# Kernel optimization log

Measured on AMD Instinct MI355X. Metric: run time of the kernel, lower is better.

The kernel has to match this reference:

```python
import jax, jax.numpy as jnp
import numpy as np


def _bilinear_sample(im, pt):
    """torch.nn.functional.grid_sample(im[None], pt[None,None], align_corners=False),
    bilinear, zeros padding.  im: (C,H,W); pt: (N,2) with (x,y) in [-1,1].
    Returns (C, N)."""
    C, H, W = im.shape
    # align_corners=False unnormalization
    x = ((pt[:, 0] + 1.0) * W - 1.0) * 0.5
    y = ((pt[:, 1] + 1.0) * H - 1.0) * 0.5
    x0 = jnp.floor(x)
    y0 = jnp.floor(y)
    wx1 = x - x0
    wy1 = y - y0
    wx0 = 1.0 - wx1
    wy0 = 1.0 - wy1
    x0i = x0.astype(jnp.int32)
    y0i = y0.astype(jnp.int32)

    def gather(xi, yi):
        inb = ((xi >= 0) & (xi < W) & (yi >= 0) & (yi < H)).astype(im.dtype)
        v = im[:, jnp.clip(yi, 0, H - 1), jnp.clip(xi, 0, W - 1)]  # (C, N)
        return v * inb

    return (gather(x0i, y0i) * (wx0 * wy0)
            + gather(x0i + 1, y0i) * (wx1 * wy0)
            + gather(x0i, y0i + 1) * (wx0 * wy1)
            + gather(x0i + 1, y0i + 1) * (wx1 * wy1))


def setup_inputs() -> dict:
    key = jax.random.key(0)
    H = W = 2048
    N = 262144
    k1, k2, k3 = jax.random.split(key, 3)
    dP = jax.random.normal(k1, (2, H, W), dtype=jnp.float32)
    inds = jnp.stack([jax.random.randint(k2, (N,), 0, H),
                      jax.random.randint(k3, (N,), 0, W)]).astype(jnp.int32)
    return {"dP": dP, "inds": inds, "niter": 60}


def reference(dP, inds, niter):
    # Faithful jax port of follow_flows + set_pt (cellpose flow integration).
    ndim, H, W = dP.shape
    # img_size_minus_1, indexed per channel k as in the original code
    sizes = jnp.array([H - 1, W - 1], dtype=jnp.float32)
    # im[0, ndim-1-n] = dP[n]; then im[:, k] *= 2 / sizes[k]
    im = dP[::-1] * (2.0 / sizes)[:, None, None]  # (2, H, W)
    # pt[..., ndim-1-n] = inds[n]  ->  pt[:, 0] = x = inds[1], pt[:, 1] = y = inds[0]
    pt0 = jnp.stack([inds[1].astype(jnp.float32),
                     inds[0].astype(jnp.float32)], axis=-1)  # (N, 2)
    pt0 = pt0 / sizes[None, :] * 2.0 - 1.0

    def step(pt, _):
        dPt = _bilinear_sample(im, pt)                 # (2, N); channel k adds to pt[..., k]
        return jnp.clip(pt + dPt.T, -1.0, 1.0), None

    pt, _ = jax.lax.scan(step, pt0, None, length=niter)
    pt = (pt + 1.0) * 0.5 * sizes[None, :]
    # return pt[..., [1, 0]].squeeze().T  -> (2, N): row0 = y, row1 = x
    return pt[:, ::-1].T
```

## Files before the change

kernel.cpp:

```cpp
#include <hip/hip_runtime.h>

#define TILE_SHIFT 5
#define NXCD 8

__global__ __launch_bounds__(256) void interleave_kernel(
    const float* __restrict__ dP, float2* __restrict__ im,
    int HW, float s0, float s1, int swz_on)
{
    int bid = blockIdx.x;
    if (swz_on) {
        int cpx = gridDim.x >> 3;
        bid = (bid & (NXCD - 1)) * cpx + (bid >> 3);
    }
    int i = bid * blockDim.x + threadIdx.x;
    int nquad = HW >> 2;
    if (i >= nquad) return;
    const float4* p0 = reinterpret_cast<const float4*>(dP);
    const float4* p1 = reinterpret_cast<const float4*>(dP + HW);
    float4 a = p1[i];
    float4 b = p0[i];
    float4 lo, hi;
    lo.x = a.x * s0; lo.y = b.x * s1; lo.z = a.y * s0; lo.w = b.y * s1;
    hi.x = a.z * s0; hi.y = b.z * s1; hi.z = a.w * s0; hi.w = b.w * s1;
    float4* outv = reinterpret_cast<float4*>(im);
    outv[2 * i]     = lo;
    outv[2 * i + 1] = hi;
}

__global__ __launch_bounds__(256) void zero_kernel(int* __restrict__ p, int n)
{
    int i = blockIdx.x * blockDim.x + threadIdx.x;
    if (i < n) p[i] = 0;
}

__device__ __forceinline__ int point_tile(const int* inds, int n, int N,
                                          int H, int W, int tiles_x)
{
    int y = inds[n];
    int x = inds[N + n];
    int ty = min(max(y, 0), H - 1) >> TILE_SHIFT;
    int tx = min(max(x, 0), W - 1) >> TILE_SHIFT;
    return ty * tiles_x + tx;
}

__global__ __launch_bounds__(256) void hist_kernel(
    const int* __restrict__ inds, int* __restrict__ hist,
    int N, int H, int W, int tiles_x)
{
    int n = blockIdx.x * blockDim.x + threadIdx.x;
    if (n >= N) return;
    atomicAdd(&hist[point_tile(inds, n, N, H, W, tiles_x)], 1);
}

__global__ __launch_bounds__(1024) void scan_kernel(
    const int* __restrict__ hist, int* __restrict__ cursor, int ntiles)
{
    __shared__ int partial[1024];
    const int tid = threadIdx.x;
    const int items = (ntiles + 1023) >> 10;
    const int base = tid * items;
    int sum = 0;
    for (int i = 0; i < items; ++i) {
        int idx = base + i;
        if (idx < ntiles) sum += hist[idx];
    }
    partial[tid] = sum;
    __syncthreads();
    for (int off = 1; off < 1024; off <<= 1) {
        int v = (tid >= off) ? partial[tid - off] : 0;
        __syncthreads();
        partial[tid] += v;
        __syncthreads();
    }
    int excl = (tid == 0) ? 0 : partial[tid - 1];
    for (int i = 0; i < items; ++i) {
        int idx = base + i;
        if (idx < ntiles) {
            int h = hist[idx];
            cursor[idx] = excl;
            excl += h;
        }
    }
}

__global__ __launch_bounds__(256) void scatter_kernel(
    const int* __restrict__ inds, int* __restrict__ cursor,
    int* __restrict__ perm, int N, int H, int W, int tiles_x)
{
    int n = blockIdx.x * blockDim.x + threadIdx.x;
    if (n >= N) return;
    int slot = atomicAdd(&cursor[point_tile(inds, n, N, H, W, tiles_x)], 1);
    perm[slot] = n;
}

template <int MODE>
__global__ __launch_bounds__(256) void iterate1_kernel(
    const float2* __restrict__ im, const float* __restrict__ dP,
    const int* __restrict__ perm,
    const int* __restrict__ inds, const int* __restrict__ niter_p,
    float* __restrict__ out, int H, int W, int N, int swz_on)
{
#pragma clang fp contract(off)
    int bid = blockIdx.x;
    if (swz_on) {
        int cpx = gridDim.x >> 3;
        bid = (bid & (NXCD - 1)) * cpx + (bid >> 3);
    }
    const int t = bid * blockDim.x + threadIdx.x;
    if (t >= N) return;
    const int niter = niter_p[0];
    const float sH = (float)(H - 1);
    const float sW = (float)(W - 1);
    const float s0 = 2.0f / sH;
    const float s1 = 2.0f / sW;
    const int HW = H * W;
    const float Wf = (float)W, Hf = (float)H;

    const int pid = (MODE == 2) ? perm[t] : t;

    float px = ((float)inds[N + pid] / sH) * 2.0f - 1.0f;
    float py = ((float)inds[pid]     / sW) * 2.0f - 1.0f;

    for (int it = 0; it < niter; ++it) {
        float x = ((px + 1.0f) * Wf - 1.0f) * 0.5f;
        float y = ((py + 1.0f) * Hf - 1.0f) * 0.5f;
        float x0f = floorf(x), y0f = floorf(y);
        float wx1 = x - x0f,  wy1 = y - y0f;
        float wx0 = 1.0f - wx1, wy0 = 1.0f - wy1;
        int x0 = (int)x0f, y0 = (int)y0f;
        int x1 = x0 + 1,   y1 = y0 + 1;

        int x0c = min(max(x0, 0), W - 1);
        int x1c = min(max(x1, 0), W - 1);
        int y0c = min(max(y0, 0), H - 1);
        int y1c = min(max(y1, 0), H - 1);
        bool bx0 = (x0 >= 0) & (x0 < W);
        bool bx1 = (x1 >= 0) & (x1 < W);
        bool by0 = (y0 >= 0) & (y0 < H);
        bool by1 = (y1 >= 0) & (y1 < H);

        float2 v00, v10, v01, v11;
        if (MODE >= 1) {
            const float2* r0 = im + (size_t)y0c * W;
            const float2* r1 = im + (size_t)y1c * W;
            v00 = r0[x0c]; v10 = r0[x1c];
            v01 = r1[x0c]; v11 = r1[x1c];
        } else {
            int i00 = y0c * W + x0c, i10 = y0c * W + x1c;
            int i01 = y1c * W + x0c, i11 = y1c * W + x1c;
            v00 = make_float2(dP[HW + i00] * s0, dP[i00] * s1);
            v10 = make_float2(dP[HW + i10] * s0, dP[i10] * s1);
            v01 = make_float2(dP[HW + i01] * s0, dP[i01] * s1);
            v11 = make_float2(dP[HW + i11] * s0, dP[i11] * s1);
        }
        const float2 zero = make_float2(0.0f, 0.0f);
        if (!(bx0 & by0)) v00 = zero;
        if (!(bx1 & by0)) v10 = zero;
        if (!(bx0 & by1)) v01 = zero;
        if (!(bx1 & by1)) v11 = zero;

        float w00 = wx0 * wy0, w10 = wx1 * wy0;
        float w01 = wx0 * wy1, w11 = wx1 * wy1;
        float dx = ((v00.x * w00 + v10.x * w10) + v01.x * w01) + v11.x * w11;
        float dy = ((v00.y * w00 + v10.y * w10) + v01.y * w01) + v11.y * w11;

        px = fminf(fmaxf(px + dx, -1.0f), 1.0f);
        py = fminf(fmaxf(py + dy, -1.0f), 1.0f);
    }

    out[pid]     = (py + 1.0f) * 0.5f * sW;
    out[N + pid] = (px + 1.0f) * 0.5f * sH;
}

extern "C" void kernel_launch(void* const* d_in, const int* in_sizes, int n_in,
                              void* d_out, int out_size, void* d_ws, size_t ws_size,
                              hipStream_t stream) {
    const float* dP      = (const float*)d_in[0];
    const int*   inds    = (const int*)d_in[1];
    const int*   niter_p = (const int*)d_in[2];
    float*       out     = (float*)d_out;

    const int HW = in_sizes[0] / 2;
    int W = 1;
    while ((long long)W * W < (long long)HW) W <<= 1;
    const int H = HW / W;
    const int N = in_sizes[1] / 2;

    const float s0 = 2.0f / (float)(H - 1);
    const float s1 = 2.0f / (float)(W - 1);

    const int tiles_x = ((W - 1) >> TILE_SHIFT) + 1;
    const int tiles_y = ((H - 1) >> TILE_SHIFT) + 1;
    const int ntiles  = tiles_x * tiles_y;

    const size_t im_bytes   = (size_t)HW * sizeof(float2);
    const size_t perm_bytes = (size_t)N * sizeof(int);
    const size_t aux_bytes  = (size_t)2 * ntiles * sizeof(int);

    char* base = (char*)d_ws;
    float2* im     = (float2*)base;
    int*    perm   = (int*)(base + im_bytes);
    int*    hist   = (int*)(base + im_bytes + perm_bytes);
    int*    cursor = hist + ntiles;

    const int nblkN  = (N + 255) / 256;
    const int nblkIm = (HW / 4 + 255) / 256;
    const int swzIm  = (nblkIm % NXCD) == 0 && (HW / 4) % 256 == 0;
    const int swzIt  = (nblkN % NXCD) == 0 && (N % 256) == 0;

    if (ws_size >= im_bytes + perm_bytes + aux_bytes) {
        interleave_kernel<<<nblkIm, 256, 0, stream>>>(
            dP, im, HW, s0, s1, swzIm);
        zero_kernel<<<(ntiles + 255) / 256, 256, 0, stream>>>(hist, ntiles);
        hist_kernel<<<nblkN, 256, 0, stream>>>(inds, hist, N, H, W, tiles_x);
        scan_kernel<<<1, 1024, 0, stream>>>(hist, cursor, ntiles);
        scatter_kernel<<<nblkN, 256, 0, stream>>>(inds, cursor, perm, N, H, W, tiles_x);
        iterate1_kernel<2><<<nblkN, 256, 0, stream>>>(
            im, dP, perm, inds, niter_p, out, H, W, N, swzIt);
    } else if (ws_size >= im_bytes) {
        interleave_kernel<<<nblkIm, 256, 0, stream>>>(
            dP, im, HW, s0, s1, swzIm);
        iterate1_kernel<1><<<nblkN, 256, 0, stream>>>(
            im, dP, nullptr, inds, niter_p, out, H, W, N, 0);
    } else {
        iterate1_kernel<0><<<nblkN, 256, 0, stream>>>(
            nullptr, dP, nullptr, inds, niter_p, out, H, W, N, 0);
    }
}
```

Before: 231.3 us.

## Stage Morton-ordered quad windows in LDS for per-block flow integration

Bins points by Morton-ordered 32x32 tiles so each group of four tiles forms a contiguous 64x64 quad in perm. One block per quad loads a 64x64 window plus a 12-pixel margin of the interleaved flow field into LDS and iterates its points from there, falling back to global memory when a sample leaves the window. This aims to replace scattered global/L2 gathers with LDS reads. The cost is an uneven per-block workload (points per quad vary, 256 threads loop over them), a large LDS allocation that limits occupancy, and divergent global fallbacks for points that drift far.

```diff
diff --git a/kernel.cpp b/kernel.cpp
--- a/kernel.cpp
+++ b/kernel.cpp
@@ -2,6 +2,9 @@
 
 #define TILE_SHIFT 5
 #define NXCD 8
+#define QUAD 64
+#define MARGIN 12
+#define LDSF2 8064
 
 __global__ __launch_bounds__(256) void interleave_kernel(
     const float* __restrict__ dP, float2* __restrict__ im,
@@ -33,23 +36,43 @@
     if (i < n) p[i] = 0;
 }
 
-__device__ __forceinline__ int point_tile(const int* inds, int n, int N,
-                                          int H, int W, int tiles_x)
+__device__ __forceinline__ unsigned part1by1(unsigned x)
+{
+    x &= 0xFFFFu;
+    x = (x | (x << 8)) & 0x00FF00FFu;
+    x = (x | (x << 4)) & 0x0F0F0F0Fu;
+    x = (x | (x << 2)) & 0x33333333u;
+    x = (x | (x << 1)) & 0x55555555u;
+    return x;
+}
+__device__ __forceinline__ unsigned compact1by1(unsigned x)
+{
+    x &= 0x55555555u;
+    x = (x | (x >> 1)) & 0x33333333u;
+    x = (x | (x >> 2)) & 0x0F0F0F0Fu;
+    x = (x | (x >> 4)) & 0x00FF00FFu;
+    x = (x | (x >> 8)) & 0x0000FFFFu;
+    return x;
+}
+
+__device__ __forceinline__ int point_bin(const int* inds, int n, int N,
+                                         int H, int W, int tiles_x, int use_morton)
 {
     int y = inds[n];
     int x = inds[N + n];
     int ty = min(max(y, 0), H - 1) >> TILE_SHIFT;
     int tx = min(max(x, 0), W - 1) >> TILE_SHIFT;
+    if (use_morton) return (int)(part1by1((unsigned)tx) | (part1by1((unsigned)ty) << 1));
     return ty * tiles_x + tx;
 }
 
 __global__ __launch_bounds__(256) void hist_kernel(
     const int* __restrict__ inds, int* __restrict__ hist,
-    int N, int H, int W, int tiles_x)
+    int N, int H, int W, int tiles_x, int use_morton)
 {
     int n = blockIdx.x * blockDim.x + threadIdx.x;
     if (n >= N) return;
-    atomicAdd(&hist[point_tile(inds, n, N, H, W, tiles_x)], 1);
+    atomicAdd(&hist[point_bin(inds, n, N, H, W, tiles_x, use_morton)], 1);
 }
 
 __global__ __launch_bounds__(1024) void scan_kernel(
@@ -85,28 +108,116 @@
 
 __global__ __launch_bounds__(256) void scatter_kernel(
     const int* __restrict__ inds, int* __restrict__ cursor,
-    int* __restrict__ perm, int N, int H, int W, int tiles_x)
+    int* __restrict__ perm, int N, int H, int W, int tiles_x, int use_morton)
 {
     int n = blockIdx.x * blockDim.x + threadIdx.x;
     if (n >= N) return;
-    int slot = atomicAdd(&cursor[point_tile(inds, n, N, H, W, tiles_x)], 1);
+    int slot = atomicAdd(&cursor[point_bin(inds, n, N, H, W, tiles_x, use_morton)], 1);
     perm[slot] = n;
+}
+
+__global__ __launch_bounds__(256) void iterate_quad_kernel(
+    const float2* __restrict__ im, const int* __restrict__ cursor,
+    const int* __restrict__ perm, const int* __restrict__ inds,
+    const int* __restrict__ niter_p, float* __restrict__ out,
+    int H, int W, int N)
+{
+#pragma clang fp contract(off)
+    __shared__ float2 win[LDSF2];
+    const int q = blockIdx.x;
+    const int qx = (int)compact1by1((unsigned)q);
+    const int qy = (int)compact1by1((unsigned)q >> 1);
+    const int wx0 = max(qx * QUAD - MARGIN, 0);
+    const int wy0 = max(qy * QUAD - MARGIN, 0);
+    const int wx1 = min(qx * QUAD + QUAD + MARGIN, W);
+    const int wy1 = min(qy * QUAD + QUAD + MARGIN, H);
+    const int wcols = wx1 - wx0, wrows = wy1 - wy0;
+    const int nwin = wcols * wrows;
+
+    {
+        int idx = threadIdx.x;
+        int r = idx / wcols;
+        int c = idx - r * wcols;
+        while (idx < nwin) {
+            win[idx] = im[(size_t)(wy0 + r) * W + wx0 + c];
+            idx += 256;
+            c += 256;
+            while (c >= wcols) { c -= wcols; ++r; }
+        }
+    }
+    __syncthreads();
+
+    const int start = (q == 0) ? 0 : cursor[4 * q - 1];
+    const int end   = cursor[4 * q + 3];
+    const int niter = niter_p[0];
+    const float sH = (float)(H - 1);
+    const float sW = (float)(W - 1);
+    const float Wf = (float)W, Hf = (float)H;
+
+    for (int s = start + (int)threadIdx.x; s < end; s += 256) {
+        const int pid = perm[s];
+        float px = ((float)inds[N + pid] / sH) * 2.0f - 1.0f;
+        float py = ((float)inds[pid]     / sW) * 2.0f - 1.0f;
+
+        for (int it = 0; it < niter; ++it) {
+            float x = ((px + 1.0f) * Wf - 1.0f) * 0.5f;
+            float y = ((py + 1.0f) * Hf - 1.0f) * 0.5f;
+            float x0f = floorf(x), y0f = floorf(y);
+            float wx1f = x - x0f,  wy1f = y - y0f;
+            float wx0f = 1.0f - wx1f, wy0f = 1.0f - wy1f;
+            int x0 = (int)x0f, y0 = (int)y0f;
+            int x1 = x0 + 1,   y1 = y0 + 1;
+
+            int x0c = min(max(x0, 0), W - 1);
+            int x1c = min(max(x1, 0), W - 1);
+            int y0c = min(max(y0, 0), H - 1);
+            int y1c = min(max(y1, 0), H - 1);
+            bool bx0 = (x0 >= 0) & (x0 < W);
+            bool bx1 = (x1 >= 0) & (x1 < W);
+            bool by0 = (y0 >= 0) & (y0 < H);
+            bool by1 = (y1 >= 0) & (y1 < H);
+
+            float2 v00, v10, v01, v11;
+            bool inwin = (x0c >= wx0) & (x1c < wx1) & (y0c >= wy0) & (y1c < wy1);
+            if (inwin) {
+                int cx0 = x0c - wx0, cx1 = x1c - wx0;
+                int ry0 = (y0c - wy0) * wcols, ry1 = (y1c - wy0) * wcols;
+                v00 = win[ry0 + cx0]; v10 = win[ry0 + cx1];
+                v01 = win[ry1 + cx0]; v11 = win[ry1 + cx1];
+            } else {
+                const float2* r0 = im + (size_t)y0c * W;
+                const float2* r1 = im + (size_t)y1c * W;
+                v00 = r0[x0c]; v10 = r0[x1c];
+                v01 = r1[x0c]; v11 = r1[x1c];
+            }
+            const float2 zero = make_float2(0.0f, 0.0f);
+            if (!(bx0 & by0)) v00 = zero;
+            if (!(bx1 & by0)) v10 = zero;
+            if (!(bx0 & by1)) v01 = zero;
+            if (!(bx1 & by1)) v11 = zero;
+
+            float w00 = wx0f * wy0f, w10 = wx1f * wy0f;
+            float w01 = wx0f * wy1f, w11 = wx1f * wy1f;
+            float dx = ((v00.x * w00 + v10.x * w10) + v01.x * w01) + v11.x * w11;
+            float dy = ((v00.y * w00 + v10.y * w10) + v01.y * w01) + v11.y * w11;
+
+            px = fminf(fmaxf(px + dx, -1.0f), 1.0f);
+            py = fminf(fmaxf(py + dy, -1.0f), 1.0f);
+        }
+
+        out[pid]     = (py + 1.0f) * 0.5f * sW;
+        out[N + pid] = (px + 1.0f) * 0.5f * sH;
+    }
 }
 
 template <int MODE>
 __global__ __launch_bounds__(256) void iterate1_kernel(
     const float2* __restrict__ im, const float* __restrict__ dP,
-    const int* __restrict__ perm,
     const int* __restrict__ inds, const int* __restrict__ niter_p,
-    float* __restrict__ out, int H, int W, int N, int swz_on)
+    float* __restrict__ out, int H, int W, int N)
 {
 #pragma clang fp contract(off)
-    int bid = blockIdx.x;
-    if (swz_on) {
-        int cpx = gridDim.x >> 3;
-        bid = (bid & (NXCD - 1)) * cpx + (bid >> 3);
-    }
-    const int t = bid * blockDim.x + threadIdx.x;
+    const int t = blockIdx.x * blockDim.x + threadIdx.x;
     if (t >= N) return;
     const int niter = niter_p[0];
     const float sH = (float)(H - 1);
@@ -116,10 +227,8 @@
     const int HW = H * W;
     const float Wf = (float)W, Hf = (float)H;
 
-    const int pid = (MODE == 2) ? perm[t] : t;
-
-    float px = ((float)inds[N + pid] / sH) * 2.0f - 1.0f;
-    float py = ((float)inds[pid]     / sW) * 2.0f - 1.0f;
+    float px = ((float)inds[N + t] / sH) * 2.0f - 1.0f;
+    float py = ((float)inds[t]     / sW) * 2.0f - 1.0f;
 
     for (int it = 0; it < niter; ++it) {
         float x = ((px + 1.0f) * Wf - 1.0f) * 0.5f;
@@ -168,8 +277,8 @@
         py = fminf(fmaxf(py + dy, -1.0f), 1.0f);
     }
 
-    out[pid]     = (py + 1.0f) * 0.5f * sW;
-    out[N + pid] = (px + 1.0f) * 0.5f * sH;
+    out[t]     = (py + 1.0f) * 0.5f * sW;
+    out[N + t] = (px + 1.0f) * 0.5f * sH;
 }
 
 extern "C" void kernel_launch(void* const* d_in, const int* in_sizes, int n_in,
@@ -193,6 +302,10 @@
     const int tiles_y = ((H - 1) >> TILE_SHIFT) + 1;
     const int ntiles  = tiles_x * tiles_y;
 
+    const bool quadOK = (tiles_x == tiles_y) && (tiles_x >= 2) &&
+                        ((tiles_x & (tiles_x - 1)) == 0);
+    const int nquads = quadOK ? (tiles_x >> 1) * (tiles_y >> 1) : 0;
+
     const size_t im_bytes   = (size_t)HW * sizeof(float2);
     const size_t perm_bytes = (size_t)N * sizeof(int);
     const size_t aux_bytes  = (size_t)2 * ntiles * sizeof(int);
@@ -206,24 +319,21 @@
     const int nblkN  = (N + 255) / 256;
     const int nblkIm = (HW / 4 + 255) / 256;
     const int swzIm  = (nblkIm % NXCD) == 0 && (HW / 4) % 256 == 0;
-    const int swzIt  = (nblkN % NXCD) == 0 && (N % 256) == 0;
-
-    if (ws_size >= im_bytes + perm_bytes + aux_bytes) {
-        interleave_kernel<<<nblkIm, 256, 0, stream>>>(
-            dP, im, HW, s0, s1, swzIm);
+
+    if (quadOK && ws_size >= im_bytes + perm_bytes + aux_bytes) {
+        interleave_kernel<<<nblkIm, 256, 0, stream>>>(dP, im, HW, s0, s1, swzIm);
         zero_kernel<<<(ntiles + 255) / 256, 256, 0, stream>>>(hist, ntiles);
-        hist_kernel<<<nblkN, 256, 0, stream>>>(inds, hist, N, H, W, tiles_x);
+        hist_kernel<<<nblkN, 256, 0, stream>>>(inds, hist, N, H, W, tiles_x, 1);
         scan_kernel<<<1, 1024, 0, stream>>>(hist, cursor, ntiles);
-        scatter_kernel<<<nblkN, 256, 0, stream>>>(inds, cursor, perm, N, H, W, tiles_x);
-        iterate1_kernel<2><<<nblkN, 256, 0, stream>>>(
-            im, dP, perm, inds, niter_p, out, H, W, N, swzIt);
+        scatter_kernel<<<nblkN, 256, 0, stream>>>(inds, cursor, perm, N, H, W, tiles_x, 1);
+        iterate_quad_kernel<<<nquads, 256, 0, stream>>>(
+            im, cursor, perm, inds, niter_p, out, H, W, N);
     } else if (ws_size >= im_bytes) {
-        interleave_kernel<<<nblkIm, 256, 0, stream>>>(
-            dP, im, HW, s0, s1, swzIm);
+        interleave_kernel<<<nblkIm, 256, 0, stream>>>(dP, im, HW, s0, s1, swzIm);
         iterate1_kernel<1><<<nblkN, 256, 0, stream>>>(
-            im, dP, nullptr, inds, niter_p, out, H, W, N, 0);
+            im, dP, inds, niter_p, out, H, W, N);
     } else {
         iterate1_kernel<0><<<nblkN, 256, 0, stream>>>(
-            nullptr, dP, nullptr, inds, niter_p, out, H, W, N, 0);
-    }
-}
+            nullptr, dP, inds, niter_p, out, H, W, N);
+    }
+}
```

Result: slower. 241.4 us (+4.4%).

## Fuse preprocessing, tile sort and iteration into one cooperative kernel

Applied to the files above, without the earlier changes.

Replaces the six-kernel sequence (interleave, zero, histogram, scan, scatter, iterate) with a single cooperative launch that separates the phases with grid-wide syncs. The goal is to remove per-launch overhead and the idle gaps between small kernels. The scan now runs on one 256-thread block instead of 1024 threads. The fused kernel only runs if all 1024 blocks can be co-resident; if the cooperative launch fails, the code falls back to the old path.

```diff
diff --git a/kernel.cpp b/kernel.cpp
--- a/kernel.cpp
+++ b/kernel.cpp
@@ -1,7 +1,160 @@
 #include <hip/hip_runtime.h>
+#include <hip/hip_cooperative_groups.h>
+
+namespace cg = cooperative_groups;
 
 #define TILE_SHIFT 5
 #define NXCD 8
+
+
+__device__ __forceinline__ int point_tile_rm(const int* inds, int n, int N,
+                                             int H, int W, int tiles_x)
+{
+    int y = inds[n];
+    int x = inds[N + n];
+    int ty = min(max(y, 0), H - 1) >> TILE_SHIFT;
+    int tx = min(max(x, 0), W - 1) >> TILE_SHIFT;
+    return ty * tiles_x + tx;
+}
+
+__global__ __launch_bounds__(256) void fused_kernel(
+    const float* __restrict__ dP, float2* __restrict__ im,
+    int* __restrict__ perm, int* __restrict__ hist, int* __restrict__ cursor,
+    const int* __restrict__ inds, const int* __restrict__ niter_p,
+    float* __restrict__ out, int H, int W, int N, int HW)
+{
+#pragma clang fp contract(off)
+    cg::grid_group grid = cg::this_grid();
+    const int tid  = threadIdx.x;
+    const int bid  = blockIdx.x;
+    const int nblk = gridDim.x;
+    const int gtid = bid * 256 + tid;
+    const int gsize = nblk * 256;
+
+    const int cpx  = nblk >> 3;
+    const int sbid = (bid & (NXCD - 1)) * cpx + (bid >> 3);
+
+    const float sH = (float)(H - 1);
+    const float sW = (float)(W - 1);
+    const float s0 = 2.0f / sH;
+    const float s1 = 2.0f / sW;
+    const int tiles_x = ((W - 1) >> TILE_SHIFT) + 1;
+    const int tiles_y = ((H - 1) >> TILE_SHIFT) + 1;
+    const int ntiles  = tiles_x * tiles_y;
+
+    {
+        const int nquad   = HW >> 2;
+        const int per_blk = nquad / nblk;
+        const int base    = sbid * per_blk;
+        const float4* p0 = reinterpret_cast<const float4*>(dP);
+        const float4* p1 = reinterpret_cast<const float4*>(dP + HW);
+        float4* outv = reinterpret_cast<float4*>(im);
+        for (int j = tid; j < per_blk; j += 256) {
+            int i = base + j;
+            float4 a = p1[i];
+            float4 b = p0[i];
+            float4 lo, hi;
+            lo.x = a.x * s0; lo.y = b.x * s1; lo.z = a.y * s0; lo.w = b.y * s1;
+            hi.x = a.z * s0; hi.y = b.z * s1; hi.z = a.w * s0; hi.w = b.w * s1;
+            outv[2 * i]     = lo;
+            outv[2 * i + 1] = hi;
+        }
+    }
+    for (int i = gtid; i < ntiles; i += gsize) hist[i] = 0;
+    grid.sync();
+
+    if (gtid < N)
+        atomicAdd(&hist[point_tile_rm(inds, gtid, N, H, W, tiles_x)], 1);
+    grid.sync();
+
+    if (bid == 0) {
+        __shared__ int partial[256];
+        const int items = (ntiles + 255) >> 8;
+        const int basei = tid * items;
+        int sum = 0;
+        for (int i = 0; i < items; ++i) {
+            int idx = basei + i;
+            if (idx < ntiles) sum += hist[idx];
+        }
+        partial[tid] = sum;
+        __syncthreads();
+        for (int off = 1; off < 256; off <<= 1) {
+            int v = (tid >= off) ? partial[tid - off] : 0;
+            __syncthreads();
+            partial[tid] += v;
+            __syncthreads();
+        }
+        int excl = (tid == 0) ? 0 : partial[tid - 1];
+        for (int i = 0; i < items; ++i) {
+            int idx = basei + i;
+            if (idx < ntiles) {
+                int h = hist[idx];
+                cursor[idx] = excl;
+                excl += h;
+            }
+        }
+    }
+    grid.sync();
+
+    if (gtid < N) {
+        int slot = atomicAdd(&cursor[point_tile_rm(inds, gtid, N, H, W, tiles_x)], 1);
+        perm[slot] = gtid;
+    }
+    grid.sync();
+
+    {
+        const int t = sbid * 256 + tid;
+        if (t < N) {
+            const int pid = perm[t];
+            const int niter = niter_p[0];
+            const float Wf = (float)W, Hf = (float)H;
+
+            float px = ((float)inds[N + pid] / sH) * 2.0f - 1.0f;
+            float py = ((float)inds[pid]     / sW) * 2.0f - 1.0f;
+
+            for (int it = 0; it < niter; ++it) {
+                float x = ((px + 1.0f) * Wf - 1.0f) * 0.5f;
+                float y = ((py + 1.0f) * Hf - 1.0f) * 0.5f;
+                float x0f = floorf(x), y0f = floorf(y);
+                float wx1 = x - x0f,  wy1 = y - y0f;
+                float wx0 = 1.0f - wx1, wy0 = 1.0f - wy1;
+                int x0 = (int)x0f, y0 = (int)y0f;
+                int x1 = x0 + 1,   y1 = y0 + 1;
+
+                int x0c = min(max(x0, 0), W - 1);
+                int x1c = min(max(x1, 0), W - 1);
+                int y0c = min(max(y0, 0), H - 1);
+                int y1c = min(max(y1, 0), H - 1);
+                bool bx0 = (x0 >= 0) & (x0 < W);
+                bool bx1 = (x1 >= 0) & (x1 < W);
+                bool by0 = (y0 >= 0) & (y0 < H);
+                bool by1 = (y1 >= 0) & (y1 < H);
+
+                const float2* r0 = im + (size_t)y0c * W;
+                const float2* r1 = im + (size_t)y1c * W;
+                float2 v00 = r0[x0c], v10 = r0[x1c];
+                float2 v01 = r1[x0c], v11 = r1[x1c];
+
+                const float2 zero = make_float2(0.0f, 0.0f);
+                if (!(bx0 & by0)) v00 = zero;
+                if (!(bx1 & by0)) v10 = zero;
+                if (!(bx0 & by1)) v01 = zero;
+                if (!(bx1 & by1)) v11 = zero;
+
+                float w00 = wx0 * wy0, w10 = wx1 * wy0;
+                float w01 = wx0 * wy1, w11 = wx1 * wy1;
+                float dx = ((v00.x * w00 + v10.x * w10) + v01.x * w01) + v11.x * w11;
+                float dy = ((v00.y * w00 + v10.y * w10) + v01.y * w01) + v11.y * w11;
+
+                px = fminf(fmaxf(px + dx, -1.0f), 1.0f);
+                py = fminf(fmaxf(py + dy, -1.0f), 1.0f);
+            }
+
+            out[pid]     = (py + 1.0f) * 0.5f * sW;
+            out[N + pid] = (px + 1.0f) * 0.5f * sH;
+        }
+    }
+}
 
 __global__ __launch_bounds__(256) void interleave_kernel(
     const float* __restrict__ dP, float2* __restrict__ im,
@@ -33,23 +186,13 @@
     if (i < n) p[i] = 0;
 }
 
-__device__ __forceinline__ int point_tile(const int* inds, int n, int N,
-                                          int H, int W, int tiles_x)
-{
-    int y = inds[n];
-    int x = inds[N + n];
-    int ty = min(max(y, 0), H - 1) >> TILE_SHIFT;
-    int tx = min(max(x, 0), W - 1) >> TILE_SHIFT;
-    return ty * tiles_x + tx;
-}
-
 __global__ __launch_bounds__(256) void hist_kernel(
     const int* __restrict__ inds, int* __restrict__ hist,
     int N, int H, int W, int tiles_x)
 {
     int n = blockIdx.x * blockDim.x + threadIdx.x;
     if (n >= N) return;
-    atomicAdd(&hist[point_tile(inds, n, N, H, W, tiles_x)], 1);
+    atomicAdd(&hist[point_tile_rm(inds, n, N, H, W, tiles_x)], 1);
 }
 
 __global__ __launch_bounds__(1024) void scan_kernel(
@@ -89,7 +232,7 @@
 {
     int n = blockIdx.x * blockDim.x + threadIdx.x;
     if (n >= N) return;
-    int slot = atomicAdd(&cursor[point_tile(inds, n, N, H, W, tiles_x)], 1);
+    int slot = atomicAdd(&cursor[point_tile_rm(inds, n, N, H, W, tiles_x)], 1);
     perm[slot] = n;
 }
 
@@ -208,9 +351,25 @@
     const int swzIm  = (nblkIm % NXCD) == 0 && (HW / 4) % 256 == 0;
     const int swzIt  = (nblkN % NXCD) == 0 && (N % 256) == 0;
 
-    if (ws_size >= im_bytes + perm_bytes + aux_bytes) {
-        interleave_kernel<<<nblkIm, 256, 0, stream>>>(
-            dP, im, HW, s0, s1, swzIm);
+    const bool sortOK = ws_size >= im_bytes + perm_bytes + aux_bytes;
+    const bool coopOK = sortOK && (N % 256 == 0) && (nblkN % NXCD) == 0 &&
+                        ((HW / 4) % nblkN) == 0 && nblkN <= 2048;
+
+    if (coopOK) {
+        int Hh = H, Ww = W, Nn = N, HWw = HW;
+        void* dPv = (void*)dP; void* imv = (void*)im; void* permv = (void*)perm;
+        void* histv = (void*)hist; void* curv = (void*)cursor;
+        void* indsv = (void*)inds; void* nitv = (void*)niter_p; void* outv = (void*)out;
+        void* args[] = { &dPv, &imv, &permv, &histv, &curv, &indsv, &nitv, &outv,
+                         &Hh, &Ww, &Nn, &HWw };
+        hipError_t e = hipLaunchCooperativeKernel(
+            (const void*)fused_kernel, dim3(nblkN), dim3(256), args, 0, stream);
+        if (e == hipSuccess) return;
+        (void)hipGetLastError();
+    }
+
+    if (sortOK) {
+        interleave_kernel<<<nblkIm, 256, 0, stream>>>(dP, im, HW, s0, s1, swzIm);
         zero_kernel<<<(ntiles + 255) / 256, 256, 0, stream>>>(hist, ntiles);
         hist_kernel<<<nblkN, 256, 0, stream>>>(inds, hist, N, H, W, tiles_x);
         scan_kernel<<<1, 1024, 0, stream>>>(hist, cursor, ntiles);
@@ -218,8 +377,7 @@
         iterate1_kernel<2><<<nblkN, 256, 0, stream>>>(
             im, dP, perm, inds, niter_p, out, H, W, N, swzIt);
     } else if (ws_size >= im_bytes) {
-        interleave_kernel<<<nblkIm, 256, 0, stream>>>(
-            dP, im, HW, s0, s1, swzIm);
+        interleave_kernel<<<nblkIm, 256, 0, stream>>>(dP, im, HW, s0, s1, swzIm);
         iterate1_kernel<1><<<nblkN, 256, 0, stream>>>(
             im, dP, nullptr, inds, niter_p, out, H, W, N, 0);
     } else {
```

Result: slower. 666.3 us (+188.1%).
